# Performance work log

Hardware: AMD Instinct MI355X
Metric: run time of the kernel (lower is better)

Reference implementation:

```python
import jax, jax.numpy as jnp
import numpy as np

EPS = 1e-5

def conv(x, w, b, stride, pad):
    y = jax.lax.conv_general_dilated(x, w, (stride, stride), [(pad, pad), (pad, pad)],
                                     dimension_numbers=('NCHW', 'OIHW', 'NCHW'))
    return y + b[None, :, None, None]

def inorm(x):
    # InstanceNorm2d, affine=False, eps=1e-5, biased variance over H,W
    m = x.mean(axis=(2, 3), keepdims=True)
    v = ((x - m) ** 2).mean(axis=(2, 3), keepdims=True)
    return (x - m) * jax.lax.rsqrt(v + EPS)

def setup_inputs() -> dict:
    key = jax.random.key(0)
    ks = jax.random.split(key, 24)
    B = 64
    x = jax.random.normal(ks[0], (B, 5, 256, 192), dtype=jnp.float32)
    chans = [(5, 8), (8, 16), (16, 32), (32, 64), (64, 128), (128, 256)]
    params = {'x': x}
    for i, (ci, co) in enumerate(chans):
        fan = ci * 16
        params[f'w{i}'] = jax.random.normal(ks[1 + 2 * i], (co, ci, 4, 4), jnp.float32) / np.sqrt(fan)
        params[f'b{i}'] = jnp.zeros((co,), jnp.float32)
    for i in (6, 7):
        params[f'w{i}'] = jax.random.normal(ks[1 + 2 * i], (256, 256, 3, 3), jnp.float32) / np.sqrt(256 * 9)
        params[f'b{i}'] = jnp.zeros((256,), jnp.float32)
    params['fc1_w'] = jax.random.normal(ks[20], (128, 512), jnp.float32) / np.sqrt(512)
    params['fc1_b'] = jnp.zeros((128,), jnp.float32)
    # fc2: weight zeroed at init in original; use small random for a nontrivial baseline
    params['fc2_w'] = jax.random.normal(ks[21], (50, 128), jnp.float32) * 0.01
    lin = np.linspace(-0.9, 0.9, 5, dtype=np.float32)
    yy, xx = np.meshgrid(lin, lin, indexing='ij')
    tcp = np.stack([xx.ravel(), yy.ravel()], axis=1)  # [25,2]
    params['fc2_b'] = jnp.asarray(np.arctanh(tcp).reshape(-1))  # [50]
    return params

def reference(x, w0, b0, w1, b1, w2, b2, w3, b3, w4, b4, w5, b5, w6, b6, w7, b7,
              fc1_w, fc1_b, fc2_w, fc2_b):
    B = x.shape[0]
    # block 0: conv -> relu -> instance_norm
    h = inorm(jax.nn.relu(conv(x, w0, b0, 2, 1)))
    # blocks 1..5: conv -> instance_norm -> relu, stride 2
    for w, b in ((w1, b1), (w2, b2), (w3, b3), (w4, b4), (w5, b5)):
        h = jax.nn.relu(inorm(conv(h, w, b, 2, 1)))
    # two 3x3 stride-1 blocks
    for w, b in ((w6, b6), (w7, b7)):
        h = jax.nn.relu(inorm(conv(h, w, b, 1, 1)))
    # maxpool 2x2 stride 2
    h = jax.lax.reduce_window(h, -jnp.inf, jax.lax.max, (1, 1, 2, 2), (1, 1, 2, 2), 'VALID')
    h = h.reshape(B, -1)  # [B,512]
    h = jax.nn.relu(h @ fc1_w.T + fc1_b)
    # F.dropout in eval mode = identity (reference is deterministic)
    pts = jnp.tanh(h @ fc2_w.T + fc2_b)  # [B,50]
    coor = pts.reshape(B, -1, 2)          # [B,25,2]
    grid = coor.reshape(B, 5, 5, 2)       # [B, row j, col i, (x,y)]

    # get_row: squared diffs along i, then abs second difference; stack order (j outer, i inner)
    d_row = (grid[:, :, 1:] - grid[:, :, :-1]) ** 2            # [B,5,4,2]
    row = jnp.abs(d_row[:, :, 1:] - d_row[:, :, :-1]).reshape(B, 15, 2)
    # get_col: same along j; stack order (i outer, j inner)
    gT = jnp.swapaxes(grid, 1, 2)                              # [B, i, j, 2]
    d_col = (gT[:, :, 1:] - gT[:, :, :-1]) ** 2
    col = jnp.abs(d_col[:, :, 1:] - d_col[:, :, :-1]).reshape(B, 15, 2)

    # grad_row / grad_col: curvature cross-product terms, BATCH ELEMENT 0 ONLY (as in original)
    def curv(g):  # g: [5,5,2], triplets along axis 1
        p0, p1, p2 = g[:, :-2], g[:, 1:-1], g[:, 2:]
        x0, y0 = p0[..., 0], p0[..., 1]
        x1, y1 = p1[..., 0], p1[..., 1]
        x2, y2 = p2[..., 0], p2[..., 1]
        return jnp.abs((y1 - y0) * (x1 - x2) - (y1 - y2) * (x1 - x0))  # [5,3]

    g0 = grid[0]
    rg_loss = jnp.maximum(curv(g0).sum(), 0.02)
    cg_loss = jnp.maximum(curv(jnp.swapaxes(g0, 0, 1)).sum(), 0.02)

    rx_loss = jnp.maximum(0.08, row[:, :, 0]).mean()
    ry_loss = jnp.maximum(0.08, row[:, :, 1]).mean()
    cx_loss = jnp.maximum(0.08, col[:, :, 0]).mean()
    cy_loss = jnp.maximum(0.08, col[:, :, 1]).mean()
    return (coor, rx_loss, ry_loss, cx_loss, cy_loss, rg_loss, cg_loss)
```

## Files before the change

kernel.cpp:

```cpp
#include <hip/hip_runtime.h>
#include <hip/hip_bf16.h>
#include <math.h>

#define EPS 1e-5f

template<int CIN, int COUT, int H, int W, int TPB>
__global__ __launch_bounds__(TPB) void conv42V(const float* __restrict__ in,
                                               const float* __restrict__ w,
                                               const float* __restrict__ bias,
                                               float* __restrict__ out, int relu)
{
    constexpr int OH  = H / 2, OW = W / 2;
    constexpr int NPX = OH * OW;
    constexpr int PXB = (NPX / 2) / TPB;
    constexpr int NCG = COUT / 8;

    __shared__ float sW[CIN * 8 * 16];
    __shared__ float sB[8];

    int t   = threadIdx.x;
    int bx  = blockIdx.x;
    int pxb = bx % PXB;
    int cg  = (bx / PXB) % NCG;
    int n   = bx / (PXB * NCG);

    for (int i = t; i < CIN * 128; i += TPB) {
        int ci = i >> 7;
        int r  = i & 127;
        int co = r >> 4;
        int k  = r & 15;
        sW[i] = w[((size_t)(cg * 8 + co) * CIN + ci) * 16 + k];
    }
    if (t < 8) sB[t] = bias[cg * 8 + t];
    __syncthreads();

    int px0 = (pxb * TPB + t) * 2;
    int oh  = px0 / OW;
    int ow0 = px0 % OW;
    int ih0 = oh * 2 - 1;
    int iwq = ow0 * 2;

    float acc[8][2];
#pragma unroll
    for (int j = 0; j < 8; ++j) { acc[j][0] = sB[j]; acc[j][1] = sB[j]; }

    const float* ib = in + (size_t)n * CIN * H * W;
#pragma unroll 1
    for (int ci = 0; ci < CIN; ++ci) {
        const float* plane = ib + (size_t)ci * H * W;
#pragma unroll
        for (int kh = 0; kh < 4; ++kh) {
            int ih = ih0 + kh;
            float p[6];
            if ((unsigned)ih < (unsigned)H) {
                const float* row = plane + (size_t)ih * W;
                float4 q = *(const float4*)(row + iwq);
                p[1] = q.x; p[2] = q.y; p[3] = q.z; p[4] = q.w;
                p[0] = (iwq >= 1)     ? row[iwq - 1] : 0.f;
                p[5] = (iwq + 4 < W)  ? row[iwq + 4] : 0.f;
            } else {
#pragma unroll
                for (int k2 = 0; k2 < 6; ++k2) p[k2] = 0.f;
            }
#pragma unroll
            for (int j = 0; j < 8; ++j) {
                const float4 wv = *(const float4*)(sW + (ci * 8 + j) * 16 + kh * 4);
                acc[j][0] = fmaf(p[0], wv.x, acc[j][0]);
                acc[j][0] = fmaf(p[1], wv.y, acc[j][0]);
                acc[j][0] = fmaf(p[2], wv.z, acc[j][0]);
                acc[j][0] = fmaf(p[3], wv.w, acc[j][0]);
                acc[j][1] = fmaf(p[2], wv.x, acc[j][1]);
                acc[j][1] = fmaf(p[3], wv.y, acc[j][1]);
                acc[j][1] = fmaf(p[4], wv.z, acc[j][1]);
                acc[j][1] = fmaf(p[5], wv.w, acc[j][1]);
            }
        }
    }
    float* ob = out + ((size_t)(n * COUT + cg * 8) * NPX) + px0;
#pragma unroll
    for (int j = 0; j < 8; ++j) {
        float2 v;
        v.x = acc[j][0];
        v.y = acc[j][1];
        if (relu) { v.x = fmaxf(v.x, 0.f); v.y = fmaxf(v.y, 0.f); }
        *(float2*)(ob + (size_t)j * NPX) = v;
    }
}

__global__ __launch_bounds__(256) void conv0(const float* __restrict__ in,
                                             const float* __restrict__ w,
                                             const float* __restrict__ bias,
                                             float* __restrict__ out)
{
    __shared__ float sW[5 * 8 * 16];
    __shared__ float sB[8];
    int t   = threadIdx.x;
    int n   = blockIdx.x / 24;
    int pxb = blockIdx.x % 24;
    for (int i = t; i < 640; i += 256) {
        int ci = i / 128;
        int r  = i % 128;
        int co = r / 16;
        int k  = r % 16;
        sW[i] = w[((size_t)co * 5 + ci) * 16 + k];
    }
    if (t < 8) sB[t] = bias[t];
    __syncthreads();

    int px0 = (pxb * 256 + t) * 2;
    int oh  = px0 / 96;
    int ow0 = px0 % 96;
    int ih0 = oh * 2 - 1;
    int iwq = ow0 * 2;

    float acc[8][2];
#pragma unroll
    for (int j = 0; j < 8; ++j) { acc[j][0] = sB[j]; acc[j][1] = sB[j]; }

    const float* ib = in + (size_t)n * 5 * 256 * 192;
#pragma unroll 1
    for (int ci = 0; ci < 5; ++ci) {
        const float* plane = ib + (size_t)ci * 256 * 192;
#pragma unroll
        for (int kh = 0; kh < 4; ++kh) {
            int ih = ih0 + kh;
            float p[6];
            if ((unsigned)ih < 256u) {
                const float* row = plane + (size_t)ih * 192;
                float4 q = *(const float4*)(row + iwq);
                p[1] = q.x; p[2] = q.y; p[3] = q.z; p[4] = q.w;
                p[0] = (iwq >= 1)      ? row[iwq - 1] : 0.f;
                p[5] = (iwq + 4 < 192) ? row[iwq + 4] : 0.f;
            } else {
#pragma unroll
                for (int k2 = 0; k2 < 6; ++k2) p[k2] = 0.f;
            }
#pragma unroll
            for (int j = 0; j < 8; ++j) {
                const float4 wv = *(const float4*)(sW + (ci * 8 + j) * 16 + kh * 4);
                acc[j][0] = fmaf(p[0], wv.x, acc[j][0]);
                acc[j][0] = fmaf(p[1], wv.y, acc[j][0]);
                acc[j][0] = fmaf(p[2], wv.z, acc[j][0]);
                acc[j][0] = fmaf(p[3], wv.w, acc[j][0]);
                acc[j][1] = fmaf(p[2], wv.x, acc[j][1]);
                acc[j][1] = fmaf(p[3], wv.y, acc[j][1]);
                acc[j][1] = fmaf(p[4], wv.z, acc[j][1]);
                acc[j][1] = fmaf(p[5], wv.w, acc[j][1]);
            }
        }
    }
    float* ob = out + (size_t)n * 8 * 12288 + px0;
#pragma unroll
    for (int j = 0; j < 8; ++j) {
        float2 v;
        v.x = fmaxf(acc[j][0], 0.f);
        v.y = fmaxf(acc[j][1], 0.f);
        *(float2*)(ob + (size_t)j * 12288) = v;
    }
}

__global__ __launch_bounds__(192) void conv_l3s(const float* __restrict__ in,
                                                const float* __restrict__ w,
                                                float* __restrict__ pbuf)
{
    __shared__ float sT[8 * 34 * 26];
    __shared__ float sW[8 * 8 * 16];
    int t  = threadIdx.x;
    int b  = blockIdx.x;
    int cg = b & 7;
    int s  = (b >> 3) & 3;
    int n  = b >> 5;

    const float* ib = in + ((size_t)n * 32 + s * 8) * 768;
    for (int i = t; i < 8 * 884; i += 192) {
        int ci  = i / 884;
        int r   = i % 884;
        int ihp = r / 26;
        int iwp = r % 26;
        int ih  = ihp - 1;
        int iw  = iwp - 1;
        float v = 0.f;
        if ((unsigned)ih < 32u && (unsigned)iw < 24u)
            v = ib[ci * 768 + ih * 24 + iw];
        sT[i] = v;
    }
    for (int i = t; i < 1024; i += 192) {
        int ci = i >> 7;
        int r  = i & 127;
        int j  = r >> 4;
        int k  = r & 15;
        sW[i] = w[((size_t)(cg * 8 + j) * 32 + s * 8 + ci) * 16 + k];
    }
    __syncthreads();

    int oh = t / 12, ow = t % 12;
    float acc[8];
#pragma unroll
    for (int j = 0; j < 8; ++j) acc[j] = 0.f;

#pragma unroll 1
    for (int ci = 0; ci < 8; ++ci) {
        const float* tp = sT + ci * 884 + (2 * oh) * 26 + 2 * ow;
        float p[16];
#pragma unroll
        for (int kh = 0; kh < 4; ++kh)
#pragma unroll
            for (int kw = 0; kw < 4; ++kw)
                p[kh * 4 + kw] = tp[kh * 26 + kw];
        const float* wp = sW + ci * 128;
#pragma unroll
        for (int j = 0; j < 8; ++j) {
#pragma unroll
            for (int k = 0; k < 16; ++k)
                acc[j] = fmaf(p[k], wp[j * 16 + k], acc[j]);
        }
    }
    float* pb = pbuf + (((size_t)s * 64 + n) * 64 + cg * 8) * 192 + t;
#pragma unroll
    for (int j = 0; j < 8; ++j) pb[j * 192] = acc[j];
}

__global__ __launch_bounds__(256) void reduce_norm_l3T(const float* __restrict__ pbuf,
                                                       float* __restrict__ dst_t)
{
    int gid  = blockIdx.x * blockDim.x + threadIdx.x;
    int wv   = gid >> 6;
    int lane = gid & 63;
    int n  = wv >> 6;
    int co = wv & 63;
    float tv[3];
#pragma unroll
    for (int k = 0; k < 3; ++k) {
        int i = lane + k * 64;
        float sum = 0.f;
#pragma unroll
        for (int s = 0; s < 4; ++s)
            sum += pbuf[((size_t)s * 4096 + wv) * 192 + i];
        tv[k] = sum;
    }
    float s1 = tv[0] + tv[1] + tv[2];
    float s2 = tv[0]*tv[0] + tv[1]*tv[1] + tv[2]*tv[2];
    for (int m = 32; m >= 1; m >>= 1) {
        s1 += __shfl_xor(s1, m);
        s2 += __shfl_xor(s2, m);
    }
    float mean = s1 * (1.f / 192.f);
    float var  = s2 * (1.f / 192.f) - mean * mean;
    float r = rsqrtf(var + EPS);
#pragma unroll
    for (int k = 0; k < 3; ++k) {
        int i = lane + k * 64;
        float y = fmaxf((tv[k] - mean) * r, 0.f);
        dst_t[((size_t)co * 192 + i) * 64 + n] = y;
    }
}

template<int TPB, int VPT>
__global__ void inorm_blockv(float* __restrict__ data, int relu)
{
    const int HW = TPB * VPT * 4;
    float4* p = (float4*)(data + (size_t)blockIdx.x * HW);
    float4 v[VPT];
    float s = 0.f, q = 0.f;
#pragma unroll
    for (int k = 0; k < VPT; ++k) {
        v[k] = p[threadIdx.x + k * TPB];
        s += v[k].x + v[k].y + v[k].z + v[k].w;
        q += v[k].x*v[k].x + v[k].y*v[k].y + v[k].z*v[k].z + v[k].w*v[k].w;
    }
    for (int m2 = 32; m2 >= 1; m2 >>= 1) {
        s += __shfl_xor(s, m2);
        q += __shfl_xor(q, m2);
    }
    __shared__ float ss[TPB / 64], sq[TPB / 64], sm[2];
    int wave = threadIdx.x >> 6, lane = threadIdx.x & 63;
    if (lane == 0) { ss[wave] = s; sq[wave] = q; }
    __syncthreads();
    if (threadIdx.x == 0) {
        float a = 0.f, b2 = 0.f;
#pragma unroll
        for (int k = 0; k < TPB / 64; ++k) { a += ss[k]; b2 += sq[k]; }
        float mm = a / (float)HW;
        float vv = b2 / (float)HW - mm * mm;
        sm[0] = mm; sm[1] = rsqrtf(vv + EPS);
    }
    __syncthreads();
    float m = sm[0], r = sm[1];
#pragma unroll
    for (int k = 0; k < VPT; ++k) {
        float4 y;
        y.x = (v[k].x - m) * r; y.y = (v[k].y - m) * r;
        y.z = (v[k].z - m) * r; y.w = (v[k].w - m) * r;
        if (relu) {
            y.x = fmaxf(y.x, 0.f); y.y = fmaxf(y.y, 0.f);
            y.z = fmaxf(y.z, 0.f); y.w = fmaxf(y.w, 0.f);
        }
        p[threadIdx.x + k * TPB] = y;
    }
}

__global__ __launch_bounds__(256) void conv_l4(const float* __restrict__ in_t,
                                               const float* __restrict__ w,
                                               float* __restrict__ pbuf)
{
    int t    = threadIdx.x;
    int lane = t & 63;
    int gw   = __builtin_amdgcn_readfirstlane(blockIdx.x * 4 + (t >> 6));
    int cog  = gw & 63;
    int cic  = (gw >> 6) & 7;
    int half = gw >> 9;
    int cc   = cic * 8;
    int co0  = cog * 2;
    int oh0  = half * 4;

    float acc[2][24];
#pragma unroll
    for (int j = 0; j < 2; ++j)
#pragma unroll
        for (int p = 0; p < 24; ++p) acc[j][p] = 0.f;

    const float* wp = w + ((size_t)co0 * 64 + cc) * 16;

#pragma unroll 1
    for (int ci = 0; ci < 8; ++ci) {
        const float* pl = in_t + (size_t)(cc + ci) * 192 * 64 + lane;
        float wr[2][16];
#pragma unroll
        for (int k = 0; k < 16; ++k) {
            wr[0][k] = wp[(0 * 64 + ci) * 16 + k];
            wr[1][k] = wp[(1 * 64 + ci) * 16 + k];
        }
#pragma unroll
        for (int kh = 0; kh < 4; ++kh) {
            float p[4][12];
#pragma unroll
            for (int o = 0; o < 4; ++o) {
                int ih = 2 * (oh0 + o) - 1 + kh;
                if ((unsigned)ih < 16u) {
#pragma unroll
                    for (int c = 0; c < 12; ++c)
                        p[o][c] = pl[(size_t)(ih * 12 + c) * 64];
                } else {
#pragma unroll
                    for (int c = 0; c < 12; ++c) p[o][c] = 0.f;
                }
            }
#pragma unroll
            for (int o = 0; o < 4; ++o)
#pragma unroll
                for (int ow = 0; ow < 6; ++ow) {
#pragma unroll
                    for (int kw = 0; kw < 4; ++kw) {
                        int iw = 2 * ow - 1 + kw;
                        if (iw < 0 || iw >= 12) continue;
                        float pv = p[o][iw];
                        acc[0][o * 6 + ow] = fmaf(pv, wr[0][kh * 4 + kw], acc[0][o * 6 + ow]);
                        acc[1][o * 6 + ow] = fmaf(pv, wr[1][kh * 4 + kw], acc[1][o * 6 + ow]);
                    }
                }
        }
    }

    float* pb = pbuf + ((size_t)(cic * 64 + lane) * 128 + co0) * 48 + oh0 * 6;
#pragma unroll
    for (int j = 0; j < 2; ++j) {
        float4* o4 = (float4*)(pb + j * 48);
#pragma unroll
        for (int q = 0; q < 6; ++q)
            o4[q] = make_float4(acc[j][q * 4 + 0], acc[j][q * 4 + 1],
                                acc[j][q * 4 + 2], acc[j][q * 4 + 3]);
    }
}

__global__ __launch_bounds__(256) void reduce_norm48(const float* __restrict__ pbuf,
                                                     float* __restrict__ out)
{
    int g  = blockIdx.x * blockDim.x + threadIdx.x;
    int co = g & 127;
    int n  = g >> 7;
    float s[48];
#pragma unroll
    for (int p = 0; p < 48; ++p) s[p] = 0.f;
#pragma unroll 1
    for (int c = 0; c < 8; ++c) {
        const float4* p4 = (const float4*)(pbuf + ((size_t)(c * 64 + n) * 128 + co) * 48);
#pragma unroll
        for (int q = 0; q < 12; ++q) {
            float4 a = p4[q];
            s[q * 4 + 0] += a.x; s[q * 4 + 1] += a.y;
            s[q * 4 + 2] += a.z; s[q * 4 + 3] += a.w;
        }
    }
    float m = 0.f;
#pragma unroll
    for (int p = 0; p < 48; ++p) m += s[p];
    m *= (1.f / 48.f);
    float q = 0.f;
#pragma unroll
    for (int p = 0; p < 48; ++p) { float d = s[p] - m; q += d * d; }
    q *= (1.f / 48.f);
    float r = rsqrtf(q + EPS);
    float4* o4 = (float4*)(out + ((size_t)n * 128 + co) * 48);
#pragma unroll
    for (int qq = 0; qq < 12; ++qq) {
        float4 v;
        v.x = fmaxf((s[qq * 4 + 0] - m) * r, 0.f);
        v.y = fmaxf((s[qq * 4 + 1] - m) * r, 0.f);
        v.z = fmaxf((s[qq * 4 + 2] - m) * r, 0.f);
        v.w = fmaxf((s[qq * 4 + 3] - m) * r, 0.f);
        o4[qq] = v;
    }
}

__global__ __launch_bounds__(256) void conv_l67(const float* __restrict__ in,
                                                const float* __restrict__ w,
                                                float* __restrict__ pbuf)
{
    int t    = threadIdx.x;
    int gw   = __builtin_amdgcn_readfirstlane(blockIdx.x * 4 + (t >> 6));
    int lane = t & 63;
    int cic  = gw >> 6;
    int cog  = gw & 63;
    int cc   = cic * 16;
    int co0  = cog * 4;

    float acc[4][12];
#pragma unroll
    for (int j = 0; j < 4; ++j)
#pragma unroll
        for (int p = 0; p < 12; ++p) acc[j][p] = 0.f;

    const float* ip = in + ((size_t)lane * 256 + cc) * 12;
    const float* wp = w + ((size_t)co0 * 256 + cc) * 9;

#pragma unroll 2
    for (int ci = 0; ci < 16; ++ci) {
        float p[12];
        const float4* p4 = (const float4*)(ip + ci * 12);
        float4 a0 = p4[0], a1 = p4[1], a2 = p4[2];
        p[0] = a0.x; p[1] = a0.y; p[2]  = a0.z; p[3]  = a0.w;
        p[4] = a1.x; p[5] = a1.y; p[6]  = a1.z; p[7]  = a1.w;
        p[8] = a2.x; p[9] = a2.y; p[10] = a2.z; p[11] = a2.w;
#pragma unroll
        for (int j = 0; j < 4; ++j) {
            const float* wj = wp + ((size_t)j * 256 + ci) * 9;
            float wr[9];
#pragma unroll
            for (int k = 0; k < 9; ++k) wr[k] = wj[k];
#pragma unroll
            for (int oh = 0; oh < 4; ++oh)
#pragma unroll
                for (int ow = 0; ow < 3; ++ow)
#pragma unroll
                    for (int kh = 0; kh < 3; ++kh) {
                        int ih = oh - 1 + kh;
                        if (ih < 0 || ih >= 4) continue;
#pragma unroll
                        for (int kw = 0; kw < 3; ++kw) {
                            int iw = ow - 1 + kw;
                            if (iw < 0 || iw >= 3) continue;
                            acc[j][oh * 3 + ow] =
                                fmaf(p[ih * 3 + iw], wr[kh * 3 + kw], acc[j][oh * 3 + ow]);
                        }
                    }
        }
    }

    float* pb = pbuf + ((size_t)(cic * 64 + lane) * 256 + co0) * 12;
#pragma unroll
    for (int j = 0; j < 4; ++j) {
        float4* o4 = (float4*)(pb + j * 12);
        o4[0] = make_float4(acc[j][0], acc[j][1], acc[j][2],  acc[j][3]);
        o4[1] = make_float4(acc[j][4], acc[j][5], acc[j][6],  acc[j][7]);
        o4[2] = make_float4(acc[j][8], acc[j][9], acc[j][10], acc[j][11]);
    }
}

__global__ __launch_bounds__(256) void conv_l5(const float* __restrict__ in,
                                               const float* __restrict__ w,
                                               float* __restrict__ pbuf)
{
    int t    = threadIdx.x;
    int gw   = __builtin_amdgcn_readfirstlane(blockIdx.x * 4 + (t >> 6));
    int lane = t & 63;
    int cic  = gw >> 6;
    int cog  = gw & 63;
    int cc   = cic * 8;
    int co0  = cog * 4;

    float acc[4][12];
#pragma unroll
    for (int j = 0; j < 4; ++j)
#pragma unroll
        for (int p = 0; p < 12; ++p) acc[j][p] = 0.f;

    const float* ip = in + ((size_t)lane * 128 + cc) * 48;
    const float* wp = w + ((size_t)co0 * 128 + cc) * 16;

#pragma unroll 1
    for (int ci = 0; ci < 8; ++ci) {
        float p[48];
        const float4* p4 = (const float4*)(ip + ci * 48);
#pragma unroll
        for (int q = 0; q < 12; ++q) {
            float4 a = p4[q];
            p[q * 4 + 0] = a.x; p[q * 4 + 1] = a.y; p[q * 4 + 2] = a.z; p[q * 4 + 3] = a.w;
        }
#pragma unroll
        for (int j = 0; j < 4; ++j) {
            const float* wj = wp + ((size_t)j * 128 + ci) * 16;
            float wr[16];
#pragma unroll
            for (int k = 0; k < 16; ++k) wr[k] = wj[k];
#pragma unroll
            for (int oh = 0; oh < 4; ++oh)
#pragma unroll
                for (int ow = 0; ow < 3; ++ow) {
                    int ih0 = 2 * oh - 1, iw0 = 2 * ow - 1;
#pragma unroll
                    for (int kh = 0; kh < 4; ++kh) {
                        int ih = ih0 + kh;
                        if (ih < 0 || ih >= 8) continue;
#pragma unroll
                        for (int kw = 0; kw < 4; ++kw) {
                            int iw = iw0 + kw;
                            if (iw < 0 || iw >= 6) continue;
                            acc[j][oh * 3 + ow] =
                                fmaf(p[ih * 6 + iw], wr[kh * 4 + kw], acc[j][oh * 3 + ow]);
                        }
                    }
                }
        }
    }

    float* pb = pbuf + ((size_t)(cic * 64 + lane) * 256 + co0) * 12;
#pragma unroll
    for (int j = 0; j < 4; ++j) {
        float4* o4 = (float4*)(pb + j * 12);
        o4[0] = make_float4(acc[j][0], acc[j][1], acc[j][2],  acc[j][3]);
        o4[1] = make_float4(acc[j][4], acc[j][5], acc[j][6],  acc[j][7]);
        o4[2] = make_float4(acc[j][8], acc[j][9], acc[j][10], acc[j][11]);
    }
}

__global__ __launch_bounds__(256) void reduce_norm12(const float* __restrict__ pbuf,
                                                     float* __restrict__ out)
{
    int g  = blockIdx.x * blockDim.x + threadIdx.x;
    int co = g & 255;
    int n  = g >> 8;
    float s[12];
#pragma unroll
    for (int p = 0; p < 12; ++p) s[p] = 0.f;
#pragma unroll 1
    for (int c = 0; c < 16; ++c) {
        const float4* p4 = (const float4*)(pbuf + ((size_t)(c * 64 + n) * 256 + co) * 12);
        float4 a = p4[0], b = p4[1], d = p4[2];
        s[0] += a.x; s[1] += a.y; s[2]  += a.z; s[3]  += a.w;
        s[4] += b.x; s[5] += b.y; s[6]  += b.z; s[7]  += b.w;
        s[8] += d.x; s[9] += d.y; s[10] += d.z; s[11] += d.w;
    }
    float m = 0.f;
#pragma unroll
    for (int p = 0; p < 12; ++p) m += s[p];
    m *= (1.f / 12.f);
    float q = 0.f;
#pragma unroll
    for (int p = 0; p < 12; ++p) { float d = s[p] - m; q += d * d; }
    q *= (1.f / 12.f);
    float r = rsqrtf(q + EPS);
    float* op = out + ((size_t)n * 256 + co) * 12;
    float4* o4 = (float4*)op;
    float y[12];
#pragma unroll
    for (int p = 0; p < 12; ++p) y[p] = fmaxf((s[p] - m) * r, 0.f);
    o4[0] = make_float4(y[0], y[1], y[2],  y[3]);
    o4[1] = make_float4(y[4], y[5], y[6],  y[7]);
    o4[2] = make_float4(y[8], y[9], y[10], y[11]);
}

__global__ void pool_kernel(const float* __restrict__ in, float* __restrict__ out)
{
    int idx = blockIdx.x * blockDim.x + threadIdx.x;
    if (idx >= 64 * 512) return;
    int f = idx & 511;
    int n = idx >> 9;
    int c = f >> 1;
    int h = f & 1;
    const float* p = in + (((size_t)n * 256 + c) * 4 + h * 2) * 3;
    out[idx] = fmaxf(fmaxf(p[0], p[1]), fmaxf(p[3], p[4]));
}

__global__ void fc1_kernel(const float* __restrict__ in, const float* __restrict__ w,
                           const float* __restrict__ b, float* __restrict__ out)
{
    int idx = blockIdx.x * blockDim.x + threadIdx.x;
    if (idx >= 64 * 128) return;
    int j = idx & 127;
    int n = idx >> 7;
    const float* x  = in + n * 512;
    const float* wr = w + j * 512;
    float acc = b[j];
    for (int f = 0; f < 512; ++f) acc = fmaf(x[f], wr[f], acc);
    out[idx] = fmaxf(acc, 0.f);
}

__global__ void fc2_kernel(const float* __restrict__ in, const float* __restrict__ w,
                           const float* __restrict__ b, float* __restrict__ out)
{
    int idx = blockIdx.x * blockDim.x + threadIdx.x;
    if (idx >= 64 * 50) return;
    int k = idx % 50;
    int n = idx / 50;
    const float* x  = in + n * 128;
    const float* wr = w + k * 128;
    float acc = b[k];
    for (int f = 0; f < 128; ++f) acc = fmaf(x[f], wr[f], acc);
    out[idx] = tanhf(acc);
}

__global__ void loss_kernel(const float* __restrict__ pts, float* __restrict__ out)
{
    __shared__ float acc[4][64];
    int n = threadIdx.x;
    float rx = 0.f, ry = 0.f, cx = 0.f, cy = 0.f;
    {
        const float* g = pts + n * 50;
        for (int r = 0; r < 5; ++r)
            for (int j = 0; j < 3; ++j)
                for (int d = 0; d < 2; ++d) {
                    float a0 = g[(r * 5 + j) * 2 + d];
                    float a1 = g[(r * 5 + j + 1) * 2 + d];
                    float a2 = g[(r * 5 + j + 2) * 2 + d];
                    float d0 = (a1 - a0) * (a1 - a0);
                    float d1 = (a2 - a1) * (a2 - a1);
                    float t = fmaxf(0.08f, fabsf(d1 - d0));
                    if (d == 0) rx += t; else ry += t;
                }
        for (int r = 0; r < 5; ++r)
            for (int j = 0; j < 3; ++j)
                for (int d = 0; d < 2; ++d) {
                    float a0 = g[(j * 5 + r) * 2 + d];
                    float a1 = g[((j + 1) * 5 + r) * 2 + d];
                    float a2 = g[((j + 2) * 5 + r) * 2 + d];
                    float d0 = (a1 - a0) * (a1 - a0);
                    float d1 = (a2 - a1) * (a2 - a1);
                    float t = fmaxf(0.08f, fabsf(d1 - d0));
                    if (d == 0) cx += t; else cy += t;
                }
    }
    acc[0][n] = rx; acc[1][n] = ry; acc[2][n] = cx; acc[3][n] = cy;
    __syncthreads();
    if (n == 0) {
        float s0 = 0.f, s1 = 0.f, s2 = 0.f, s3 = 0.f;
        for (int i = 0; i < 64; ++i) {
            s0 += acc[0][i]; s1 += acc[1][i]; s2 += acc[2][i]; s3 += acc[3][i];
        }
        float inv = 1.0f / (64.0f * 15.0f);
        out[3200] = s0 * inv;
        out[3201] = s1 * inv;
        out[3202] = s2 * inv;
        out[3203] = s3 * inv;
        const float* g = pts;
        float rg = 0.f, cg = 0.f;
        for (int r = 0; r < 5; ++r)
            for (int j = 0; j < 3; ++j) {
                float x0 = g[(r * 5 + j) * 2],     y0 = g[(r * 5 + j) * 2 + 1];
                float x1 = g[(r * 5 + j + 1) * 2], y1 = g[(r * 5 + j + 1) * 2 + 1];
                float x2 = g[(r * 5 + j + 2) * 2], y2 = g[(r * 5 + j + 2) * 2 + 1];
                rg += fabsf((y1 - y0) * (x1 - x2) - (y1 - y2) * (x1 - x0));
            }
        for (int r = 0; r < 5; ++r)
            for (int j = 0; j < 3; ++j) {
                float x0 = g[(j * 5 + r) * 2],       y0 = g[(j * 5 + r) * 2 + 1];
                float x1 = g[((j + 1) * 5 + r) * 2], y1 = g[((j + 1) * 5 + r) * 2 + 1];
                float x2 = g[((j + 2) * 5 + r) * 2], y2 = g[((j + 2) * 5 + r) * 2 + 1];
                cg += fabsf((y1 - y0) * (x1 - x2) - (y1 - y2) * (x1 - x0));
            }
        out[3204] = fmaxf(rg, 0.02f);
        out[3205] = fmaxf(cg, 0.02f);
    }
}

extern "C" void kernel_launch(void* const* d_in, const int* in_sizes, int n_in,
                              void* d_out, int out_size, void* d_ws, size_t ws_size,
                              hipStream_t stream)
{
    const float* x = (const float*)d_in[0];
    const float* w[8], *bia[8];
    for (int i = 0; i < 6; ++i) { w[i] = (const float*)d_in[1 + 2 * i]; bia[i] = (const float*)d_in[2 + 2 * i]; }
    w[6] = (const float*)d_in[13]; bia[6] = (const float*)d_in[14];
    w[7] = (const float*)d_in[15]; bia[7] = (const float*)d_in[16];
    const float* fc1_w = (const float*)d_in[17];
    const float* fc1_b = (const float*)d_in[18];
    const float* fc2_w = (const float*)d_in[19];
    const float* fc2_b = (const float*)d_in[20];
    float* out = (float*)d_out;

    float* A      = (float*)d_ws;
    float* Bf     = A + 6291456;
    float* pooled = Bf + 3145728;
    float* fc1o   = pooled + 32768;
    float* pbuf3  = A + 1572864;
    float* At     = A;
    float* l4out  = A + 1048576;
    float* pbuf   = A + 3145728;

    const int N = 64;

    conv0<<<1536, 256, 0, stream>>>(x, w[0], bia[0], A);
    inorm_blockv<256, 12><<<N * 8, 256, 0, stream>>>(A, 0);

    conv42V<8, 16, 128, 96, 256><<<768, 256, 0, stream>>>(A, w[1], bia[1], Bf, 0);
    inorm_blockv<256, 3><<<N * 16, 256, 0, stream>>>(Bf, 1);

    conv42V<16, 32, 64, 48, 192><<<512, 192, 0, stream>>>(Bf, w[2], bia[2], A, 0);
    inorm_blockv<192, 1><<<N * 32, 192, 0, stream>>>(A, 1);

    conv_l3s<<<2048, 192, 0, stream>>>(A, w[3], pbuf3);
    reduce_norm_l3T<<<1024, 256, 0, stream>>>(pbuf3, At);

    conv_l4<<<256, 256, 0, stream>>>(At, w[4], pbuf);
    reduce_norm48<<<32, 256, 0, stream>>>(pbuf, l4out);

    conv_l5<<<256, 256, 0, stream>>>(l4out, w[5], pbuf);
    reduce_norm12<<<64, 256, 0, stream>>>(pbuf, Bf);

    conv_l67<<<256, 256, 0, stream>>>(Bf, w[6], pbuf);
    reduce_norm12<<<64, 256, 0, stream>>>(pbuf, A);

    conv_l67<<<256, 256, 0, stream>>>(A, w[7], pbuf);
    float* l7out = Bf + 262144;
    reduce_norm12<<<64, 256, 0, stream>>>(pbuf, l7out);

    pool_kernel<<<(64 * 512 + 255) / 256, 256, 0, stream>>>(l7out, pooled);
    fc1_kernel<<<(64 * 128 + 255) / 256, 256, 0, stream>>>(pooled, fc1_w, fc1_b, fc1o);
    fc2_kernel<<<(64 * 50 + 255) / 256, 256, 0, stream>>>(fc1o, fc2_w, fc2_b, out);
    loss_kernel<<<1, 64, 0, stream>>>(out, out);
}
```

Measured before the change: 466.7 us.

## Transpose layer-2 norm output to batch-minor and rewrite layer-3 conv per-wave

The layer-2 instance norm becomes a one-wave-per-channel kernel that writes its output in a [C][HW][N] layout with batch innermost. The layer-3 conv is rewritten so that each lane handles one batch element and each wave covers one output row for two output channels over an 8-channel input slice. Weights are read with wave-uniform loads instead of being staged in shared memory. This drops the shared-memory tiling and padding work, but the transposed writes in the norm kernel are strided, and the partial-sum buffer moves to a new workspace offset.

```diff
diff --git a/kernel.cpp b/kernel.cpp
--- a/kernel.cpp
+++ b/kernel.cpp
@@ -159,65 +159,102 @@
     }
 }
 
-__global__ __launch_bounds__(192) void conv_l3s(const float* __restrict__ in,
+__global__ __launch_bounds__(256) void inorm_wave_T768(const float* __restrict__ src,
+                                                       float* __restrict__ dst_t)
+{
+    int gid  = blockIdx.x * blockDim.x + threadIdx.x;
+    int wv   = gid >> 6;
+    int lane = gid & 63;
+    int n = wv >> 5;
+    int c = wv & 31;
+    const float* p = src + (size_t)wv * 768;
+    float tv[12];
+    float s1 = 0.f, s2 = 0.f;
+#pragma unroll
+    for (int k = 0; k < 12; ++k) {
+        float v = p[lane + k * 64];
+        tv[k] = v;
+        s1 += v; s2 += v * v;
+    }
+    for (int m = 32; m >= 1; m >>= 1) {
+        s1 += __shfl_xor(s1, m);
+        s2 += __shfl_xor(s2, m);
+    }
+    float mean = s1 * (1.f / 768.f);
+    float var  = s2 * (1.f / 768.f) - mean * mean;
+    float r = rsqrtf(var + EPS);
+#pragma unroll
+    for (int k = 0; k < 12; ++k) {
+        int i = lane + k * 64;
+        float y = fmaxf((tv[k] - mean) * r, 0.f);
+        dst_t[((size_t)c * 768 + i) * 64 + n] = y;
+    }
+}
+
+__global__ __launch_bounds__(256) void conv_l3t(const float* __restrict__ in_t,
                                                 const float* __restrict__ w,
                                                 float* __restrict__ pbuf)
 {
-    __shared__ float sT[8 * 34 * 26];
-    __shared__ float sW[8 * 8 * 16];
-    int t  = threadIdx.x;
-    int b  = blockIdx.x;
-    int cg = b & 7;
-    int s  = (b >> 3) & 3;
-    int n  = b >> 5;
-
-    const float* ib = in + ((size_t)n * 32 + s * 8) * 768;
-    for (int i = t; i < 8 * 884; i += 192) {
-        int ci  = i / 884;
-        int r   = i % 884;
-        int ihp = r / 26;
-        int iwp = r % 26;
-        int ih  = ihp - 1;
-        int iw  = iwp - 1;
-        float v = 0.f;
-        if ((unsigned)ih < 32u && (unsigned)iw < 24u)
-            v = ib[ci * 768 + ih * 24 + iw];
-        sT[i] = v;
-    }
-    for (int i = t; i < 1024; i += 192) {
-        int ci = i >> 7;
-        int r  = i & 127;
-        int j  = r >> 4;
-        int k  = r & 15;
-        sW[i] = w[((size_t)(cg * 8 + j) * 32 + s * 8 + ci) * 16 + k];
-    }
-    __syncthreads();
-
-    int oh = t / 12, ow = t % 12;
-    float acc[8];
-#pragma unroll
-    for (int j = 0; j < 8; ++j) acc[j] = 0.f;
+    int t    = threadIdx.x;
+    int lane = t & 63;
+    int gw   = __builtin_amdgcn_readfirstlane(blockIdx.x * 4 + (t >> 6));
+    int cog  = gw & 31;
+    int cic  = (gw >> 5) & 3;
+    int oh   = gw >> 7;
+    int cc   = cic * 8;
+    int co0  = cog * 2;
+    int ih0  = 2 * oh - 1;
+
+    float acc[2][12];
+#pragma unroll
+    for (int j = 0; j < 2; ++j)
+#pragma unroll
+        for (int p = 0; p < 12; ++p) acc[j][p] = 0.f;
+
+    const float* wb = w + ((size_t)co0 * 32 + cc) * 16;
 
 #pragma unroll 1
     for (int ci = 0; ci < 8; ++ci) {
-        const float* tp = sT + ci * 884 + (2 * oh) * 26 + 2 * ow;
-        float p[16];
-#pragma unroll
-        for (int kh = 0; kh < 4; ++kh)
-#pragma unroll
-            for (int kw = 0; kw < 4; ++kw)
-                p[kh * 4 + kw] = tp[kh * 26 + kw];
-        const float* wp = sW + ci * 128;
-#pragma unroll
-        for (int j = 0; j < 8; ++j) {
-#pragma unroll
-            for (int k = 0; k < 16; ++k)
-                acc[j] = fmaf(p[k], wp[j * 16 + k], acc[j]);
-        }
-    }
-    float* pb = pbuf + (((size_t)s * 64 + n) * 64 + cg * 8) * 192 + t;
-#pragma unroll
-    for (int j = 0; j < 8; ++j) pb[j * 192] = acc[j];
+        const float* pl = in_t + (size_t)(cc + ci) * 768 * 64 + lane;
+        float wr[2][16];
+#pragma unroll
+        for (int k = 0; k < 16; ++k) {
+            wr[0][k] = wb[(0 * 32 + ci) * 16 + k];
+            wr[1][k] = wb[(1 * 32 + ci) * 16 + k];
+        }
+#pragma unroll
+        for (int kh = 0; kh < 4; ++kh) {
+            int ih = ih0 + kh;
+            float p[26];
+            p[0] = 0.f; p[25] = 0.f;
+            if ((unsigned)ih < 32u) {
+#pragma unroll
+                for (int c = 0; c < 24; ++c)
+                    p[c + 1] = pl[(size_t)(ih * 24 + c) * 64];
+            } else {
+#pragma unroll
+                for (int c = 0; c < 24; ++c) p[c + 1] = 0.f;
+            }
+#pragma unroll
+            for (int ow = 0; ow < 12; ++ow) {
+#pragma unroll
+                for (int kw = 0; kw < 4; ++kw) {
+                    float pv = p[2 * ow + kw];
+                    acc[0][ow] = fmaf(pv, wr[0][kh * 4 + kw], acc[0][ow]);
+                    acc[1][ow] = fmaf(pv, wr[1][kh * 4 + kw], acc[1][ow]);
+                }
+            }
+        }
+    }
+
+    float* pb = pbuf + ((size_t)cic * 4096 + (size_t)lane * 64 + co0) * 192 + oh * 12;
+#pragma unroll
+    for (int j = 0; j < 2; ++j) {
+        float4* o4 = (float4*)(pb + (size_t)j * 192);
+        o4[0] = make_float4(acc[j][0], acc[j][1], acc[j][2],  acc[j][3]);
+        o4[1] = make_float4(acc[j][4], acc[j][5], acc[j][6],  acc[j][7]);
+        o4[2] = make_float4(acc[j][8], acc[j][9], acc[j][10], acc[j][11]);
+    }
 }
 
 __global__ __launch_bounds__(256) void reduce_norm_l3T(const float* __restrict__ pbuf,
@@ -701,7 +738,8 @@
     float* Bf     = A + 6291456;
     float* pooled = Bf + 3145728;
     float* fc1o   = pooled + 32768;
-    float* pbuf3  = A + 1572864;
+    float* At2    = A + 1572864;
+    float* pbuf3  = A + 3145728;
     float* At     = A;
     float* l4out  = A + 1048576;
     float* pbuf   = A + 3145728;
@@ -715,9 +753,9 @@
     inorm_blockv<256, 3><<<N * 16, 256, 0, stream>>>(Bf, 1);
 
     conv42V<16, 32, 64, 48, 192><<<512, 192, 0, stream>>>(Bf, w[2], bia[2], A, 0);
-    inorm_blockv<192, 1><<<N * 32, 192, 0, stream>>>(A, 1);
-
-    conv_l3s<<<2048, 192, 0, stream>>>(A, w[3], pbuf3);
+    inorm_wave_T768<<<512, 256, 0, stream>>>(A, At2);
+
+    conv_l3t<<<512, 256, 0, stream>>>(At2, w[3], pbuf3);
     reduce_norm_l3T<<<1024, 256, 0, stream>>>(pbuf3, At);
 
     conv_l4<<<256, 256, 0, stream>>>(At, w[4], pbuf);
```

Result: faster. 423.3 us (-9.3%).
